# Kernel optimization log

Hardware: AMD Instinct MI355X
Metric: run time of the kernel (lower is better)

The kernel has to match this reference:

```python
import jax, jax.numpy as jnp
import numpy as np

SIZE = 1024
CODE_DIM = 256
B, H, W = 32, 32, 32


def setup_inputs() -> dict:
    key = jax.random.key(0)
    k1, k2 = jax.random.split(key)
    z = jax.random.normal(k1, (B, CODE_DIM, H, W), dtype=jnp.float32)
    embeddings = jax.random.normal(k2, (SIZE, CODE_DIM), dtype=jnp.float32)
    return {"z": z, "embeddings": embeddings}


def reference(z, embeddings):
    b, c, h, w = z.shape  # c == code_dim
    # (b, h, w, c) -> (N, c)
    flat = jnp.transpose(z, (0, 2, 3, 1)).reshape(-1, c)
    d = (
        jnp.sum(flat * flat, axis=-1, keepdims=True)
        - 2.0 * (flat @ embeddings.T)
        + jnp.sum(embeddings * embeddings, axis=-1)
    )
    idx = jnp.argmin(d, axis=-1)  # (N,)
    quantized = embeddings[idx].reshape(b, h, w, c)
    quantized = jnp.transpose(quantized, (0, 3, 1, 2))  # (b, c, h, w)
    straight_through = jax.lax.stop_gradient(quantized - z) + z
    return quantized, straight_through, idx.reshape(b, h, w)
```

## Files before the change

kernel.cpp:

```cpp
#include <hip/hip_runtime.h>

#define NPTS   32768
#define NCODES 1024
#define DIM    256
#define HWSZ   1024
#define CHW    (DIM*HWSZ)
#define QSZ    8388608

typedef __attribute__((ext_vector_type(8))) short short8;
typedef __attribute__((ext_vector_type(4))) float f32x4;

__device__ __forceinline__ void gload16(const void* g, void* l) {
    __builtin_amdgcn_global_load_lds((const __attribute__((address_space(1))) void*)g,
                                     (__attribute__((address_space(3))) void*)l,
                                     16, 0, 0);
}

__device__ __forceinline__ unsigned bf16_rne(float f) {
    unsigned u = __float_as_uint(f);
    return (u + 0x7fffu + ((u >> 16) & 1u)) >> 16;
}

__global__ void k_prep_e(const float* __restrict__ emb, short* __restrict__ Eh,
                         short* __restrict__ El, float* __restrict__ e2) {
    int tid = threadIdx.x, lane = tid & 63, w = tid >> 6;
    int k = blockIdx.x * 4 + w;
    const float4 v = *reinterpret_cast<const float4*>(emb + k * DIM + lane * 4);
    float f[4] = {v.x, v.y, v.z, v.w};
    short h[4], l[4];
    double s = 0.0;
    #pragma unroll
    for (int i = 0; i < 4; ++i) {
        unsigned hb = bf16_rne(f[i]);
        float hf = __uint_as_float(hb << 16);
        h[i] = (short)hb;
        l[i] = (short)bf16_rne(f[i] - hf);
        s += (double)f[i] * f[i];
    }
    *reinterpret_cast<short4*>(Eh + k * DIM + lane * 4) = make_short4(h[0], h[1], h[2], h[3]);
    *reinterpret_cast<short4*>(El + k * DIM + lane * 4) = make_short4(l[0], l[1], l[2], l[3]);
    #pragma unroll
    for (int m = 32; m >= 1; m >>= 1) s += __shfl_xor(s, m);
    if (lane == 0) e2[k] = (float)s;
}

__global__ void k_prep_x(const float* __restrict__ z, short* __restrict__ Xh,
                         short* __restrict__ Xl) {
    __shared__ float T[64][33];
    int blk = blockIdx.x;
    int b  = blk >> 5;
    int ht = blk & 31;
    int hw0 = ht * 32;
    int n0  = b * HWSZ + hw0;
    int tid = threadIdx.x;
    int hq = tid & 7, cr = tid >> 3;
    int wp = tid >> 3, wc = tid & 7;
    const float* zp = z + b * CHW;
    #pragma unroll
    for (int cc = 0; cc < 4; ++cc) {
        int c0 = cc * 64;
        if (cc) __syncthreads();
        #pragma unroll
        for (int p = 0; p < 2; ++p) {
            int c = p * 32 + cr;
            float4 v = *reinterpret_cast<const float4*>(zp + (c0 + c) * HWSZ + hw0 + hq * 4);
            T[c][hq * 4 + 0] = v.x; T[c][hq * 4 + 1] = v.y;
            T[c][hq * 4 + 2] = v.z; T[c][hq * 4 + 3] = v.w;
        }
        __syncthreads();
        short8 hv, lv;
        #pragma unroll
        for (int k = 0; k < 8; ++k) {
            float f = T[wc * 8 + k][wp];
            unsigned hb = bf16_rne(f);
            float hf = __uint_as_float(hb << 16);
            hv[k] = (short)hb;
            lv[k] = (short)bf16_rne(f - hf);
        }
        *reinterpret_cast<short8*>(Xh + (n0 + wp) * DIM + c0 + wc * 8) = hv;
        *reinterpret_cast<short8*>(Xl + (n0 + wp) * DIM + c0 + wc * 8) = lv;
    }
}

__launch_bounds__(256, 4)
__global__ void k_dist(const short* __restrict__ Xh, const short* __restrict__ Xl,
                       const short* __restrict__ Eh, const short* __restrict__ El,
                       const float* __restrict__ e2, float* __restrict__ minv,
                       int* __restrict__ mini) {
    __shared__ __align__(16) short Ah[4096];
    __shared__ __align__(16) short Al[4096];
    __shared__ __align__(16) short Bh[4096];
    __shared__ __align__(16) short Bl[4096];
    __shared__ float sv[2][128];
    __shared__ int   si[2][128];

    const int tid = threadIdx.x;
    const int pt = blockIdx.x & 255;
    const int ct = blockIdx.x >> 8;
    const int n0 = pt * 128;
    const int c0 = ct * 128;

    const int w = tid >> 6, lane = tid & 63;
    const int wr = w >> 1, wc = w & 1;
    const int m16 = lane & 15, quad = lane >> 4;

    f32x4 acc[4][4];
    #pragma unroll
    for (int i = 0; i < 4; ++i)
        #pragma unroll
        for (int j = 0; j < 4; ++j) acc[i][j] = (f32x4){0.f, 0.f, 0.f, 0.f};

    const int r  = lane >> 2;
    const int ks = (lane & 3) * 8;
    const int ldsoff0 = (w * 16) * 64;
    const int ldsoff1 = (64 + w * 16) * 64;
    const int arow0 = (n0 + w * 16 + r) * DIM;
    const int arow1 = (n0 + 64 + w * 16 + r) * DIM;
    const int brow0 = (c0 + w * 16 + r) * DIM;
    const int brow1 = (c0 + 64 + w * 16 + r) * DIM;

    for (int t = 0; t < 8; ++t) {
        const int koff = t * 32 + ks;
        __syncthreads();
        gload16(Xh + arow0 + koff, (char*)Ah + ldsoff0);
        gload16(Xh + arow1 + koff, (char*)Ah + ldsoff1);
        gload16(Xl + arow0 + koff, (char*)Al + ldsoff0);
        gload16(Xl + arow1 + koff, (char*)Al + ldsoff1);
        gload16(Eh + brow0 + koff, (char*)Bh + ldsoff0);
        gload16(Eh + brow1 + koff, (char*)Bh + ldsoff1);
        gload16(El + brow0 + koff, (char*)Bl + ldsoff0);
        gload16(El + brow1 + koff, (char*)Bl + ldsoff1);
        __syncthreads();

        short8 ah[4], al[4], bh[4], bl[4];
        #pragma unroll
        for (int i = 0; i < 4; ++i) {
            int ar = (wr * 64 + i * 16 + m16) * 32 + quad * 8;
            ah[i] = *(const short8*)&Ah[ar];
            al[i] = *(const short8*)&Al[ar];
        }
        #pragma unroll
        for (int j = 0; j < 4; ++j) {
            int br = (wc * 64 + j * 16 + m16) * 32 + quad * 8;
            bh[j] = *(const short8*)&Bh[br];
            bl[j] = *(const short8*)&Bl[br];
        }
        #pragma unroll
        for (int i = 0; i < 4; ++i)
            #pragma unroll
            for (int j = 0; j < 4; ++j)
                acc[i][j] = __builtin_amdgcn_mfma_f32_16x16x32_bf16(ah[i], bh[j], acc[i][j], 0, 0, 0);
        #pragma unroll
        for (int i = 0; i < 4; ++i)
            #pragma unroll
            for (int j = 0; j < 4; ++j)
                acc[i][j] = __builtin_amdgcn_mfma_f32_16x16x32_bf16(al[i], bh[j], acc[i][j], 0, 0, 0);
        #pragma unroll
        for (int i = 0; i < 4; ++i)
            #pragma unroll
            for (int j = 0; j < 4; ++j)
                acc[i][j] = __builtin_amdgcn_mfma_f32_16x16x32_bf16(ah[i], bl[j], acc[i][j], 0, 0, 0);
    }

    float ecol[4];
    #pragma unroll
    for (int j = 0; j < 4; ++j) ecol[j] = e2[c0 + wc * 64 + j * 16 + m16];

    #pragma unroll
    for (int i = 0; i < 4; ++i) {
        #pragma unroll
        for (int rr = 0; rr < 4; ++rr) {
            float best = 3.4e38f; int bi = 0;
            #pragma unroll
            for (int j = 0; j < 4; ++j) {
                float d = fmaf(-2.f, acc[i][j][rr], ecol[j]);
                int code = c0 + wc * 64 + j * 16 + m16;
                if (d < best) { best = d; bi = code; }
            }
            #pragma unroll
            for (int m = 1; m < 16; m <<= 1) {
                float ov = __shfl_xor(best, m);
                int   oi = __shfl_xor(bi, m);
                if (ov < best || (ov == best && oi < bi)) { best = ov; bi = oi; }
            }
            if (m16 == 0) {
                int p = wr * 64 + i * 16 + quad * 4 + rr;
                sv[wc][p] = best; si[wc][p] = bi;
            }
        }
    }
    __syncthreads();
    if (tid < 128) {
        float v0 = sv[0][tid]; int i0 = si[0][tid];
        float v1 = sv[1][tid]; int i1 = si[1][tid];
        if (v1 < v0) { v0 = v1; i0 = i1; }
        minv[ct * NPTS + n0 + tid] = v0;
        mini[ct * NPTS + n0 + tid] = i0;
    }
}

__global__ void k_out(const float* __restrict__ z, const float* __restrict__ emb,
                      const float* __restrict__ minv, const int* __restrict__ mini,
                      float* __restrict__ out) {
    __shared__ float Q[32][257];
    __shared__ int sbi[32];
    int n0 = blockIdx.x * 32;
    int tid = threadIdx.x;
    if (tid < 32) {
        int n = n0 + tid;
        float bv = minv[n]; int bi = mini[n];
        #pragma unroll
        for (int g = 1; g < 8; ++g) {
            float v = minv[g * NPTS + n]; int ii = mini[g * NPTS + n];
            if (v < bv) { bv = v; bi = ii; }
        }
        sbi[tid] = bi;
        out[2 * QSZ + n] = (float)bi;
    }
    __syncthreads();
    {
        int pt = tid >> 3, co = tid & 7;
        const float* ep = emb + sbi[pt] * DIM;
        #pragma unroll
        for (int j = 0; j < 8; ++j) {
            int c = j * 32 + co * 4;
            float4 v = *reinterpret_cast<const float4*>(ep + c);
            Q[pt][c] = v.x; Q[pt][c + 1] = v.y; Q[pt][c + 2] = v.z; Q[pt][c + 3] = v.w;
        }
    }
    __syncthreads();
    int hq = tid & 7, cr = tid >> 3;
    int b = n0 >> 10, hw0 = (n0 & 1023) + hq * 4;
    #pragma unroll
    for (int it = 0; it < 8; ++it) {
        int c = it * 32 + cr;
        int off = b * CHW + c * HWSZ + hw0;
        float4 zv = *reinterpret_cast<const float4*>(z + off);
        float4 q = make_float4(Q[hq * 4 + 0][c], Q[hq * 4 + 1][c],
                               Q[hq * 4 + 2][c], Q[hq * 4 + 3][c]);
        *reinterpret_cast<float4*>(out + off) = q;
        float4 st = make_float4((q.x - zv.x) + zv.x, (q.y - zv.y) + zv.y,
                                (q.z - zv.z) + zv.z, (q.w - zv.w) + zv.w);
        *reinterpret_cast<float4*>(out + QSZ + off) = st;
    }
}

extern "C" void kernel_launch(void* const* d_in, const int* in_sizes, int n_in,
                              void* d_out, int out_size, void* d_ws, size_t ws_size,
                              hipStream_t stream) {
    const float* z   = (const float*)d_in[0];
    const float* emb = (const float*)d_in[1];
    float* out = (float*)d_out;
    float* ws  = (float*)d_ws;

    short* Eh   = (short*)ws;
    short* El   = (short*)(ws + 131072);
    float* e2   = ws + 262144;
    float* minv = ws + 263168;
    int*   mini = (int*)(ws + 525312);

    short* Xh = (short*)out;
    short* Xl = (short*)(out + 4194304);

    hipLaunchKernelGGL(k_prep_e, dim3(256),  dim3(256), 0, stream, emb, Eh, El, e2);
    hipLaunchKernelGGL(k_prep_x, dim3(1024), dim3(256), 0, stream, z, Xh, Xl);
    hipLaunchKernelGGL(k_dist,   dim3(2048), dim3(256), 0, stream, Xh, Xl, Eh, El, e2, minv, mini);
    hipLaunchKernelGGL(k_out,    dim3(1024), dim3(256), 0, stream, z, emb, minv, mini, out);
}
```

Baseline: 167.9 us.

## Merge prep kernels and give each wave a 64x128 distance tile with swizzled LDS

The two prep kernels become one launch, with extra blocks handling the embedding split. The distance kernel now runs two waves per block, each computing 64 points by 128 codes. This removes the cross-wave argmin reduction through LDS and lets each B fragment load feed more MFMAs. Each wave loads either the hi or the lo halves, with an XOR-style swizzle of the K offset meant to cut LDS bank conflicts. The trade-off is double the accumulator registers (128 floats) and fewer waves per block, which may lower occupancy and latency hiding.

```diff
diff --git a/kernel.cpp b/kernel.cpp
--- a/kernel.cpp
+++ b/kernel.cpp
@@ -21,38 +21,39 @@
     return (u + 0x7fffu + ((u >> 16) & 1u)) >> 16;
 }
 
-__global__ void k_prep_e(const float* __restrict__ emb, short* __restrict__ Eh,
-                         short* __restrict__ El, float* __restrict__ e2) {
-    int tid = threadIdx.x, lane = tid & 63, w = tid >> 6;
-    int k = blockIdx.x * 4 + w;
-    const float4 v = *reinterpret_cast<const float4*>(emb + k * DIM + lane * 4);
-    float f[4] = {v.x, v.y, v.z, v.w};
-    short h[4], l[4];
-    double s = 0.0;
-    #pragma unroll
-    for (int i = 0; i < 4; ++i) {
-        unsigned hb = bf16_rne(f[i]);
-        float hf = __uint_as_float(hb << 16);
-        h[i] = (short)hb;
-        l[i] = (short)bf16_rne(f[i] - hf);
-        s += (double)f[i] * f[i];
-    }
-    *reinterpret_cast<short4*>(Eh + k * DIM + lane * 4) = make_short4(h[0], h[1], h[2], h[3]);
-    *reinterpret_cast<short4*>(El + k * DIM + lane * 4) = make_short4(l[0], l[1], l[2], l[3]);
-    #pragma unroll
-    for (int m = 32; m >= 1; m >>= 1) s += __shfl_xor(s, m);
-    if (lane == 0) e2[k] = (float)s;
-}
-
-__global__ void k_prep_x(const float* __restrict__ z, short* __restrict__ Xh,
-                         short* __restrict__ Xl) {
+__global__ void k_prep(const float* __restrict__ z, const float* __restrict__ emb,
+                       short* __restrict__ Xh, short* __restrict__ Xl,
+                       short* __restrict__ Eh, short* __restrict__ El,
+                       float* __restrict__ e2) {
+    int tid = threadIdx.x;
+    if (blockIdx.x >= 1024) {
+        int lane = tid & 63, w = tid >> 6;
+        int k = (blockIdx.x - 1024) * 4 + w;
+        const float4 v = *reinterpret_cast<const float4*>(emb + k * DIM + lane * 4);
+        float f[4] = {v.x, v.y, v.z, v.w};
+        short h[4], l[4];
+        double s = 0.0;
+        #pragma unroll
+        for (int i = 0; i < 4; ++i) {
+            unsigned hb = bf16_rne(f[i]);
+            float hf = __uint_as_float(hb << 16);
+            h[i] = (short)hb;
+            l[i] = (short)bf16_rne(f[i] - hf);
+            s += (double)f[i] * f[i];
+        }
+        *reinterpret_cast<short4*>(Eh + k * DIM + lane * 4) = make_short4(h[0], h[1], h[2], h[3]);
+        *reinterpret_cast<short4*>(El + k * DIM + lane * 4) = make_short4(l[0], l[1], l[2], l[3]);
+        #pragma unroll
+        for (int m = 32; m >= 1; m >>= 1) s += __shfl_xor(s, m);
+        if (lane == 0) e2[k] = (float)s;
+        return;
+    }
     __shared__ float T[64][33];
     int blk = blockIdx.x;
     int b  = blk >> 5;
     int ht = blk & 31;
     int hw0 = ht * 32;
     int n0  = b * HWSZ + hw0;
-    int tid = threadIdx.x;
     int hq = tid & 7, cr = tid >> 3;
     int wp = tid >> 3, wc = tid & 7;
     const float* zp = z + b * CHW;
@@ -82,7 +83,7 @@
     }
 }
 
-__launch_bounds__(256, 4)
+__launch_bounds__(128, 2)
 __global__ void k_dist(const short* __restrict__ Xh, const short* __restrict__ Xl,
                        const short* __restrict__ Eh, const short* __restrict__ El,
                        const float* __restrict__ e2, float* __restrict__ minv,
@@ -91,8 +92,6 @@
     __shared__ __align__(16) short Al[4096];
     __shared__ __align__(16) short Bh[4096];
     __shared__ __align__(16) short Bl[4096];
-    __shared__ float sv[2][128];
-    __shared__ int   si[2][128];
 
     const int tid = threadIdx.x;
     const int pt = blockIdx.x & 255;
@@ -101,70 +100,57 @@
     const int c0 = ct * 128;
 
     const int w = tid >> 6, lane = tid & 63;
-    const int wr = w >> 1, wc = w & 1;
     const int m16 = lane & 15, quad = lane >> 4;
 
-    f32x4 acc[4][4];
+    f32x4 acc[4][8];
     #pragma unroll
     for (int i = 0; i < 4; ++i)
         #pragma unroll
-        for (int j = 0; j < 4; ++j) acc[i][j] = (f32x4){0.f, 0.f, 0.f, 0.f};
-
-    const int r  = lane >> 2;
-    const int ks = (lane & 3) * 8;
-    const int ldsoff0 = (w * 16) * 64;
-    const int ldsoff1 = (64 + w * 16) * 64;
-    const int arow0 = (n0 + w * 16 + r) * DIM;
-    const int arow1 = (n0 + 64 + w * 16 + r) * DIM;
-    const int brow0 = (c0 + w * 16 + r) * DIM;
-    const int brow1 = (c0 + 64 + w * 16 + r) * DIM;
+        for (int j = 0; j < 8; ++j) acc[i][j] = (f32x4){0.f, 0.f, 0.f, 0.f};
+
+    const int r4  = lane >> 2;
+    const int swz = (((lane & 3) - ((lane >> 3) & 3)) & 3) * 8;
+    const short* srcA = w ? Xl : Xh;
+    const short* srcB = w ? El : Eh;
+    char* dstA = (char*)(w ? Al : Ah);
+    char* dstB = (char*)(w ? Bl : Bh);
+
+    const int pq = ((quad + (m16 >> 1)) & 3) * 8;
 
     for (int t = 0; t < 8; ++t) {
-        const int koff = t * 32 + ks;
+        const int koff = t * 32 + swz;
         __syncthreads();
-        gload16(Xh + arow0 + koff, (char*)Ah + ldsoff0);
-        gload16(Xh + arow1 + koff, (char*)Ah + ldsoff1);
-        gload16(Xl + arow0 + koff, (char*)Al + ldsoff0);
-        gload16(Xl + arow1 + koff, (char*)Al + ldsoff1);
-        gload16(Eh + brow0 + koff, (char*)Bh + ldsoff0);
-        gload16(Eh + brow1 + koff, (char*)Bh + ldsoff1);
-        gload16(El + brow0 + koff, (char*)Bl + ldsoff0);
-        gload16(El + brow1 + koff, (char*)Bl + ldsoff1);
+        #pragma unroll
+        for (int g = 0; g < 8; ++g) {
+            gload16(srcA + (n0 + g * 16 + r4) * DIM + koff, dstA + g * 1024);
+            gload16(srcB + (c0 + g * 16 + r4) * DIM + koff, dstB + g * 1024);
+        }
         __syncthreads();
 
-        short8 ah[4], al[4], bh[4], bl[4];
+        short8 ah[4], al[4];
         #pragma unroll
         for (int i = 0; i < 4; ++i) {
-            int ar = (wr * 64 + i * 16 + m16) * 32 + quad * 8;
+            int ar = (w * 64 + i * 16 + m16) * 32 + pq;
             ah[i] = *(const short8*)&Ah[ar];
             al[i] = *(const short8*)&Al[ar];
         }
         #pragma unroll
-        for (int j = 0; j < 4; ++j) {
-            int br = (wc * 64 + j * 16 + m16) * 32 + quad * 8;
-            bh[j] = *(const short8*)&Bh[br];
-            bl[j] = *(const short8*)&Bl[br];
-        }
-        #pragma unroll
-        for (int i = 0; i < 4; ++i)
+        for (int j = 0; j < 8; ++j) {
+            int br = (j * 16 + m16) * 32 + pq;
+            short8 bh = *(const short8*)&Bh[br];
+            short8 bl = *(const short8*)&Bl[br];
             #pragma unroll
-            for (int j = 0; j < 4; ++j)
-                acc[i][j] = __builtin_amdgcn_mfma_f32_16x16x32_bf16(ah[i], bh[j], acc[i][j], 0, 0, 0);
-        #pragma unroll
-        for (int i = 0; i < 4; ++i)
-            #pragma unroll
-            for (int j = 0; j < 4; ++j)
-                acc[i][j] = __builtin_amdgcn_mfma_f32_16x16x32_bf16(al[i], bh[j], acc[i][j], 0, 0, 0);
-        #pragma unroll
-        for (int i = 0; i < 4; ++i)
-            #pragma unroll
-            for (int j = 0; j < 4; ++j)
-                acc[i][j] = __builtin_amdgcn_mfma_f32_16x16x32_bf16(ah[i], bl[j], acc[i][j], 0, 0, 0);
-    }
-
-    float ecol[4];
-    #pragma unroll
-    for (int j = 0; j < 4; ++j) ecol[j] = e2[c0 + wc * 64 + j * 16 + m16];
+            for (int i = 0; i < 4; ++i) {
+                acc[i][j] = __builtin_amdgcn_mfma_f32_16x16x32_bf16(ah[i], bh, acc[i][j], 0, 0, 0);
+                acc[i][j] = __builtin_amdgcn_mfma_f32_16x16x32_bf16(al[i], bh, acc[i][j], 0, 0, 0);
+                acc[i][j] = __builtin_amdgcn_mfma_f32_16x16x32_bf16(ah[i], bl, acc[i][j], 0, 0, 0);
+            }
+        }
+    }
+
+    float ecol[8];
+    #pragma unroll
+    for (int j = 0; j < 8; ++j) ecol[j] = e2[c0 + j * 16 + m16];
 
     #pragma unroll
     for (int i = 0; i < 4; ++i) {
@@ -172,9 +158,9 @@
         for (int rr = 0; rr < 4; ++rr) {
             float best = 3.4e38f; int bi = 0;
             #pragma unroll
-            for (int j = 0; j < 4; ++j) {
+            for (int j = 0; j < 8; ++j) {
                 float d = fmaf(-2.f, acc[i][j][rr], ecol[j]);
-                int code = c0 + wc * 64 + j * 16 + m16;
+                int code = c0 + j * 16 + m16;
                 if (d < best) { best = d; bi = code; }
             }
             #pragma unroll
@@ -184,18 +170,11 @@
                 if (ov < best || (ov == best && oi < bi)) { best = ov; bi = oi; }
             }
             if (m16 == 0) {
-                int p = wr * 64 + i * 16 + quad * 4 + rr;
-                sv[wc][p] = best; si[wc][p] = bi;
-            }
-        }
-    }
-    __syncthreads();
-    if (tid < 128) {
-        float v0 = sv[0][tid]; int i0 = si[0][tid];
-        float v1 = sv[1][tid]; int i1 = si[1][tid];
-        if (v1 < v0) { v0 = v1; i0 = i1; }
-        minv[ct * NPTS + n0 + tid] = v0;
-        mini[ct * NPTS + n0 + tid] = i0;
+                int n = n0 + w * 64 + i * 16 + quad * 4 + rr;
+                minv[ct * NPTS + n] = best;
+                mini[ct * NPTS + n] = bi;
+            }
+        }
     }
 }
 
@@ -262,8 +241,7 @@
     short* Xh = (short*)out;
     short* Xl = (short*)(out + 4194304);
 
-    hipLaunchKernelGGL(k_prep_e, dim3(256),  dim3(256), 0, stream, emb, Eh, El, e2);
-    hipLaunchKernelGGL(k_prep_x, dim3(1024), dim3(256), 0, stream, z, Xh, Xl);
-    hipLaunchKernelGGL(k_dist,   dim3(2048), dim3(256), 0, stream, Xh, Xl, Eh, El, e2, minv, mini);
-    hipLaunchKernelGGL(k_out,    dim3(1024), dim3(256), 0, stream, z, emb, minv, mini, out);
-}
+    hipLaunchKernelGGL(k_prep, dim3(1280), dim3(256), 0, stream, z, emb, Xh, Xl, Eh, El, e2);
+    hipLaunchKernelGGL(k_dist, dim3(2048), dim3(128), 0, stream, Xh, Xl, Eh, El, e2, minv, mini);
+    hipLaunchKernelGGL(k_out,  dim3(1024), dim3(256), 0, stream, z, emb, minv, mini, out);
+}
```

Result: slower. 175.8 us (+4.7%).
